# Kernel tuning notes

Measured on AMD Instinct MI355X. Metric: run time of the kernel, lower is better.

Reference implementation:

```python
import jax, jax.numpy as jnp
import numpy as np

D_MODEL = 256
N_HEADS = 4
D_HEAD = D_MODEL // N_HEADS
SCALE = 1.0 / np.sqrt(D_HEAD).astype(np.float32)


def setup_inputs() -> dict:
    key = jax.random.key(0)
    ks = jax.random.split(key, 8)
    B, T, S = 4, 512, 512
    return {
        "query": jax.random.normal(ks[0], (B, T, D_MODEL), dtype=jnp.float32),
        "key": jax.random.normal(ks[1], (B, S, D_MODEL), dtype=jnp.float32),
        "value": jax.random.normal(ks[2], (B, S, D_MODEL), dtype=jnp.float32),
        "w_q": jax.random.normal(ks[3], (D_MODEL, D_MODEL), dtype=jnp.float32) * 0.05,
        "w_k": jax.random.normal(ks[4], (D_MODEL, D_MODEL), dtype=jnp.float32) * 0.05,
        "w_v": jax.random.normal(ks[5], (D_MODEL, D_MODEL), dtype=jnp.float32) * 0.05,
        "v_a": jax.random.normal(ks[6], (N_HEADS, D_HEAD), dtype=jnp.float32),
        "w_o": jax.random.normal(ks[7], (D_MODEL, D_MODEL), dtype=jnp.float32) * 0.05,
    }


def reference(query, key, value, w_q, w_k, w_v, v_a, w_o):
    B, T, _ = query.shape
    S = key.shape[1]
    # projections; weights stored as (out, in) like nn.Linear -> x @ W.T
    Q = (query @ w_q.T).reshape(B, T, N_HEADS, D_HEAD).transpose(0, 2, 1, 3)  # bhtd
    K = (key @ w_k.T).reshape(B, S, N_HEADS, D_HEAD).transpose(0, 2, 1, 3)    # bhsd
    V = (value @ w_v.T).reshape(B, S, N_HEADS, D_HEAD).transpose(0, 2, 1, 3)  # bhsd
    # additive (Bahdanau) scores: tanh broadcast of shape (B,H,T,S,Dh)
    combined = jnp.tanh(Q[:, :, :, None, :] + K[:, :, None, :, :])
    scores = jnp.einsum('bhtsd,hd->bhts', combined, v_a) * SCALE
    attn = jax.nn.softmax(scores, axis=-1)  # (B,H,T,S)
    attended = jnp.einsum('bhts,bhsd->bhtd', attn, V)
    attended = attended.transpose(0, 2, 1, 3).reshape(B, T, D_MODEL)
    out = attended @ w_o.T
    return out, attn
```

## Files before the change

### kernel.cpp

```cpp
#include <hip/hip_runtime.h>
#include <math.h>

#define BATCH 4
#define TLEN 512
#define SLEN 512
#define DM 256
#define NH 4
#define DH 64
#define BT (BATCH * TLEN)

__device__ __forceinline__ float rcp_fast(float x) { return __builtin_amdgcn_rcpf(x); }

__global__ __launch_bounds__(256) void transposeN_kernel(
    const float* __restrict__ s0, const float* __restrict__ s1,
    const float* __restrict__ s2, const float* __restrict__ s3,
    float* __restrict__ d0, float* __restrict__ d1,
    float* __restrict__ d2, float* __restrict__ d3) {
  __shared__ float tile[64][65];
  int m = blockIdx.y;
  const float* S = (m == 0) ? s0 : (m == 1) ? s1 : (m == 2) ? s2 : s3;
  float* D = (m == 0) ? d0 : (m == 1) ? d1 : (m == 2) ? d2 : d3;
  int bx = blockIdx.x;
  int to = (bx & 3) * 64;
  int tk = (bx >> 2) * 64;
  int lo = threadIdx.x >> 6;
  int lk = threadIdx.x & 63;
#pragma unroll
  for (int p = 0; p < 16; ++p) {
    int o = p * 4 + lo;
    tile[o][lk] = S[(size_t)(to + o) * DM + tk + lk];
  }
  __syncthreads();
#pragma unroll
  for (int p = 0; p < 16; ++p) {
    int kk = p * 4 + lo;
    D[(size_t)(tk + kk) * DM + to + lk] = tile[lk][kk];
  }
}

__global__ __launch_bounds__(256) void proj_kernel(
    const float* __restrict__ q, const float* __restrict__ k, const float* __restrict__ v,
    const float* __restrict__ wqt, const float* __restrict__ wkt, const float* __restrict__ wvt,
    float* __restrict__ EQ, float* __restrict__ EKT, float* __restrict__ Vw) {
  int tid = threadIdx.x;
  int lane = tid & 63;
  int wid = __builtin_amdgcn_readfirstlane(tid >> 6);
  int which = blockIdx.y;
  const float* X = (which == 0) ? q : (which == 1) ? k : v;
  const float* WT = (which == 0) ? wqt : (which == 1) ? wkt : wvt;
  int row0 = (blockIdx.x >> 2) * 16 + wid * 4;
  int o = (blockIdx.x & 3) * 64 + lane;
  const float* xb = X + (size_t)row0 * DM;
  const float* wcol = WT + o;
  float a0 = 0.f, a1 = 0.f, a2 = 0.f, a3 = 0.f;
#pragma unroll 8
  for (int kk = 0; kk < DM; ++kk) {
    float w = wcol[(size_t)kk * DM];
    a0 = fmaf(xb[kk], w, a0);
    a1 = fmaf(xb[DM + kk], w, a1);
    a2 = fmaf(xb[2 * DM + kk], w, a2);
    a3 = fmaf(xb[3 * DM + kk], w, a3);
  }
  int h = o >> 6, d = o & 63;
  float accs[4] = {a0, a1, a2, a3};
#pragma unroll
  for (int r = 0; r < 4; ++r) {
    int row = row0 + r;
    int b = row >> 9, t = row & 511;
    int bh = b * NH + h;
    float val = accs[r];
    if (which < 2) {
      val = __expf(2.f * fminf(fmaxf(val, -5.5f), 5.5f));
    }
    if (which == 0) {
      EQ[((size_t)bh * TLEN + t) * DH + d] = val;
    } else if (which == 1) {
      EKT[(((size_t)bh * 16 + (d >> 2)) * SLEN + t) * 4 + (d & 3)] = val;
    } else {
      Vw[(size_t)bh * SLEN * DH + (size_t)(t >> 1) * 128 + d * 2 + (t & 1)] = val;
    }
  }
}

__global__ __launch_bounds__(256, 8) void attn_kernel(
    const float* __restrict__ EQ, const float* __restrict__ EKT,
    const float* __restrict__ Vw, const float* __restrict__ va_g,
    float* __restrict__ attn_out, float* __restrict__ attended) {
  __shared__ float pw[4][SLEN];
  __shared__ float fp[4][4][64];
  __shared__ float sred[4][4];
  int tid = threadIdx.x;
  int lane = tid & 63;
  int wid = __builtin_amdgcn_readfirstlane(tid >> 6);
  int bx = (int)((blockIdx.x & 7) * 256 + (blockIdx.x >> 3));
  int bh = bx >> 7;
  int tile = (bx & 127) * 4;
  int h = bh & 3, b = bh >> 2;
  int sq0 = wid * 128;

  const float4* ekf = (const float4*)EKT + (size_t)bh * (16 * SLEN) + sq0 + lane;
  const float* eqb = EQ + ((size_t)bh * TLEN + tile) * DH;
  const float* vap = va_g + h * DH;

  float acc[4][2];
#pragma unroll
  for (int t = 0; t < 4; ++t) { acc[t][0] = 0.f; acc[t][1] = 0.f; }
  float vsum = 0.f;

  float4 eA0, eA1, eB0, eB1;

#define LOADE(EV, dc_) do { EV##0 = ekf[(size_t)(dc_) * SLEN]; \
                            EV##1 = ekf[(size_t)(dc_) * SLEN + 64]; } while (0)

#define SC4(E, qv, av, aref) do {                                           \
    float A0 = fmaf(qv.x, E.x, 1.f), A1 = fmaf(qv.y, E.y, 1.f);             \
    float A2 = fmaf(qv.z, E.z, 1.f), A3 = fmaf(qv.w, E.w, 1.f);             \
    float n01 = fmaf(av.x, A1, av.y * A0);                                  \
    float n23 = fmaf(av.z, A3, av.w * A2);                                  \
    float P01 = A0 * A1, P23 = A2 * A3;                                     \
    float Nm = fmaf(n01, P23, n23 * P01);                                   \
    aref = fmaf(Nm, rcp_fast(P01 * P23), aref);                             \
  } while (0)

#define DCBODY(CUR, NXT, dc_) do {                                          \
    float4 av = *(const float4*)(vap + (dc_) * 4);                          \
    float4 q0 = *(const float4*)(eqb + 0 * DH + (dc_) * 4);                 \
    float4 q1 = *(const float4*)(eqb + 1 * DH + (dc_) * 4);                 \
    float4 q2 = *(const float4*)(eqb + 2 * DH + (dc_) * 4);                 \
    float4 q3 = *(const float4*)(eqb + 3 * DH + (dc_) * 4);                 \
    vsum += (av.x + av.y) + (av.z + av.w);                                  \
    if ((dc_) < 15) LOADE(NXT, (dc_) + 1);                                  \
    __builtin_amdgcn_sched_barrier(0);                                      \
    SC4(CUR##0, q0, av, acc[0][0]); SC4(CUR##1, q0, av, acc[0][1]);         \
    SC4(CUR##0, q1, av, acc[1][0]); SC4(CUR##1, q1, av, acc[1][1]);         \
    SC4(CUR##0, q2, av, acc[2][0]); SC4(CUR##1, q2, av, acc[2][1]);         \
    SC4(CUR##0, q3, av, acc[3][0]); SC4(CUR##1, q3, av, acc[3][1]);         \
  } while (0)

  LOADE(eA, 0);
#pragma unroll 1
  for (int dc2 = 0; dc2 < 8; ++dc2) {
    DCBODY(eA, eB, 2 * dc2);
    DCBODY(eB, eA, 2 * dc2 + 1);
  }

  size_t bht = (size_t)bh * TLEN + tile;
  float e0[4], e1[4];
#pragma unroll
  for (int t = 0; t < 4; ++t) {
    float x0 = __expf(fmaf(acc[t][0], -0.25f, vsum * 0.125f));
    float x1 = __expf(fmaf(acc[t][1], -0.25f, vsum * 0.125f));
    e0[t] = x0; e1[t] = x1;
    float es = x0 + x1;
#pragma unroll
    for (int off = 32; off; off >>= 1) es += __shfl_xor(es, off);
    if (lane == 0) sred[t][wid] = es;
  }
  __syncthreads();
#pragma unroll
  for (int t = 0; t < 4; ++t) {
    float es = (sred[t][0] + sred[t][1]) + (sred[t][2] + sred[t][3]);
    float inv = rcp_fast(es);
    float p0 = e0[t] * inv, p1 = e1[t] * inv;
    pw[t][sq0 + lane] = p0;
    pw[t][sq0 + 64 + lane] = p1;
    float* arow = attn_out + (bht + t) * SLEN + sq0;
    arow[lane] = p0;
    arow[64 + lane] = p1;
  }

  const float2* vb = (const float2*)Vw + (size_t)bh * (256 * 64) + (size_t)(wid * 64) * 64 + lane;
  float f[4];
#pragma unroll
  for (int t = 0; t < 4; ++t) f[t] = 0.f;
#pragma unroll 2
  for (int i = 0; i < 32; ++i) {
    float2 v01 = vb[(size_t)i * 128];
    float2 v23 = vb[(size_t)i * 128 + 64];
    int sb = sq0 + i * 4;
#pragma unroll
    for (int t = 0; t < 4; ++t) {
      float4 pq = *(const float4*)&pw[t][sb];
      f[t] = fmaf(pq.x, v01.x, f[t]);
      f[t] = fmaf(pq.y, v01.y, f[t]);
      f[t] = fmaf(pq.z, v23.x, f[t]);
      f[t] = fmaf(pq.w, v23.y, f[t]);
    }
  }
#pragma unroll
  for (int t = 0; t < 4; ++t) fp[wid][t][lane] = f[t];
  __syncthreads();
  {
    int t = wid;
    float s = (fp[0][t][lane] + fp[1][t][lane]) + (fp[2][t][lane] + fp[3][t][lane]);
    attended[((size_t)(b * TLEN) + tile + t) * DM + h * DH + lane] = s;
  }
}

__global__ __launch_bounds__(256) void outproj_kernel(
    const float* __restrict__ att, const float* __restrict__ wot,
    float* __restrict__ out) {
  int tid = threadIdx.x;
  int lane = tid & 63;
  int wid = __builtin_amdgcn_readfirstlane(tid >> 6);
  int row0 = (blockIdx.x >> 2) * 8 + wid * 2;
  int o = (blockIdx.x & 3) * 64 + lane;
  const float* xb = att + (size_t)row0 * DM;
  const float* wcol = wot + o;
  float a0 = 0.f, a1 = 0.f;
#pragma unroll 8
  for (int kk = 0; kk < DM; ++kk) {
    float w = wcol[(size_t)kk * DM];
    a0 = fmaf(xb[kk], w, a0);
    a1 = fmaf(xb[DM + kk], w, a1);
  }
  out[(size_t)(row0 + 0) * DM + o] = a0;
  out[(size_t)(row0 + 1) * DM + o] = a1;
}

extern "C" void kernel_launch(void* const* d_in, const int* in_sizes, int n_in,
                              void* d_out, int out_size, void* d_ws, size_t ws_size,
                              hipStream_t stream) {
  const float* query = (const float*)d_in[0];
  const float* key   = (const float*)d_in[1];
  const float* value = (const float*)d_in[2];
  const float* wq    = (const float*)d_in[3];
  const float* wk    = (const float*)d_in[4];
  const float* wv    = (const float*)d_in[5];
  const float* va    = (const float*)d_in[6];
  const float* wo    = (const float*)d_in[7];

  float* out  = (float*)d_out;
  float* attn = out + (size_t)BT * DM;

  const size_t SEG = (size_t)BT * DM;
  float* EQ  = (float*)d_ws;
  float* EKT = EQ + SEG;
  float* Vw  = EKT + SEG;
  float* att = Vw + SEG;

  bool big_ws = ws_size >= (4 * SEG + 4 * (size_t)DM * DM) * sizeof(float);

  if (big_ws) {
    float* WTq = att + SEG;
    float* WTk = WTq + (size_t)DM * DM;
    float* WTv = WTk + (size_t)DM * DM;
    float* WoT = WTv + (size_t)DM * DM;
    transposeN_kernel<<<dim3(16, 4), 256, 0, stream>>>(wq, wk, wv, wo, WTq, WTk, WTv, WoT);
    proj_kernel<<<dim3(512, 3), 256, 0, stream>>>(query, key, value, WTq, WTk, WTv, EQ, EKT, Vw);
    attn_kernel<<<dim3(2048), 256, 0, stream>>>(EQ, EKT, Vw, va, attn, att);
    outproj_kernel<<<dim3(1024), 256, 0, stream>>>(att, WoT, out);
  } else {
    float* WTq = att;
    float* WTk = att + (size_t)DM * DM;
    float* WTv = att + 2 * (size_t)DM * DM;
    float* WoT = EQ;
    transposeN_kernel<<<dim3(16, 3), 256, 0, stream>>>(wq, wk, wv, wv, WTq, WTk, WTv, WTv);
    proj_kernel<<<dim3(512, 3), 256, 0, stream>>>(query, key, value, WTq, WTk, WTv, EQ, EKT, Vw);
    attn_kernel<<<dim3(2048), 256, 0, stream>>>(EQ, EKT, Vw, va, attn, att);
    transposeN_kernel<<<dim3(16, 1), 256, 0, stream>>>(wo, wo, wo, wo, WoT, WoT, WoT, WoT);
    outproj_kernel<<<dim3(1024), 256, 0, stream>>>(att, WoT, out);
  }
}
```

Baseline: 87.14 us.

## Pack exp(K) pairs in interleaved layout and use packed f32x2 math in score loop

The exp(2K) tensor is now stored so that each lane's two key positions (s and s+64) sit next to each other per head-dim element. The score inner loop computes both keys together with 2-wide float vector FMAs/multiplies, targeting the packed FP32 instructions (v_pk_fma_f32, v_pk_mul_f32) available on CDNA3-class GPUs and roughly halving the VALU instruction count for that math. Reciprocals stay scalar. The trade-offs are possible register/packing overhead, since the scalar q/va values must be broadcast into both halves, and a changed global load pattern of 8-byte loads instead of float4.

```diff
diff --git a/kernel.cpp b/kernel.cpp
--- a/kernel.cpp
+++ b/kernel.cpp
@@ -9,16 +9,20 @@
 #define DH 64
 #define BT (BATCH * TLEN)
 
+typedef float f2 __attribute__((ext_vector_type(2)));
+
 __device__ __forceinline__ float rcp_fast(float x) { return __builtin_amdgcn_rcpf(x); }
+__device__ __forceinline__ f2 f2fma(f2 a, f2 b, f2 c) { return __builtin_elementwise_fma(a, b, c); }
+__device__ __forceinline__ f2 s2(float v) { f2 r; r.x = v; r.y = v; return r; }
 
 __global__ __launch_bounds__(256) void transposeN_kernel(
     const float* __restrict__ s0, const float* __restrict__ s1,
-    const float* __restrict__ s2, const float* __restrict__ s3,
+    const float* __restrict__ s2_, const float* __restrict__ s3,
     float* __restrict__ d0, float* __restrict__ d1,
     float* __restrict__ d2, float* __restrict__ d3) {
   __shared__ float tile[64][65];
   int m = blockIdx.y;
-  const float* S = (m == 0) ? s0 : (m == 1) ? s1 : (m == 2) ? s2 : s3;
+  const float* S = (m == 0) ? s0 : (m == 1) ? s1 : (m == 2) ? s2_ : s3;
   float* D = (m == 0) ? d0 : (m == 1) ? d1 : (m == 2) ? d2 : d3;
   int bx = blockIdx.x;
   int to = (bx & 3) * 64;
@@ -75,7 +79,8 @@
     if (which == 0) {
       EQ[((size_t)bh * TLEN + t) * DH + d] = val;
     } else if (which == 1) {
-      EKT[(((size_t)bh * 16 + (d >> 2)) * SLEN + t) * 4 + (d & 3)] = val;
+      int dc = d >> 2, j = d & 3, qq = t >> 7, l = t & 63, hi = (t >> 6) & 1;
+      EKT[((((size_t)bh * 16 + dc) * 4 + qq) * 64 + l) * 8 + j * 2 + hi] = val;
     } else {
       Vw[(size_t)bh * SLEN * DH + (size_t)(t >> 1) * 128 + d * 2 + (t & 1)] = val;
     }
@@ -98,58 +103,64 @@
   int h = bh & 3, b = bh >> 2;
   int sq0 = wid * 128;
 
-  const float4* ekf = (const float4*)EKT + (size_t)bh * (16 * SLEN) + sq0 + lane;
+  const float* ekb = EKT + (size_t)bh * (16 * 2048) + wid * 512 + lane * 8;
   const float* eqb = EQ + ((size_t)bh * TLEN + tile) * DH;
   const float* vap = va_g + h * DH;
 
-  float acc[4][2];
-#pragma unroll
-  for (int t = 0; t < 4; ++t) { acc[t][0] = 0.f; acc[t][1] = 0.f; }
+  f2 acc2[4];
+#pragma unroll
+  for (int t = 0; t < 4; ++t) acc2[t] = s2(0.f);
   float vsum = 0.f;
 
-  float4 eA0, eA1, eB0, eB1;
-
-#define LOADE(EV, dc_) do { EV##0 = ekf[(size_t)(dc_) * SLEN]; \
-                            EV##1 = ekf[(size_t)(dc_) * SLEN + 64]; } while (0)
-
-#define SC4(E, qv, av, aref) do {                                           \
-    float A0 = fmaf(qv.x, E.x, 1.f), A1 = fmaf(qv.y, E.y, 1.f);             \
-    float A2 = fmaf(qv.z, E.z, 1.f), A3 = fmaf(qv.w, E.w, 1.f);             \
-    float n01 = fmaf(av.x, A1, av.y * A0);                                  \
-    float n23 = fmaf(av.z, A3, av.w * A2);                                  \
-    float P01 = A0 * A1, P23 = A2 * A3;                                     \
-    float Nm = fmaf(n01, P23, n23 * P01);                                   \
-    aref = fmaf(Nm, rcp_fast(P01 * P23), aref);                             \
+  f2 a0_, a1_, a2_, a3_, b0_, b1_, b2_, b3_;
+
+#define LOADP(E0, E1, E2, E3, dc_) do {                                     \
+    const f2* _p = (const f2*)(ekb + (size_t)(dc_) * 2048);                 \
+    E0 = _p[0]; E1 = _p[1]; E2 = _p[2]; E3 = _p[3];                         \
   } while (0)
 
-#define DCBODY(CUR, NXT, dc_) do {                                          \
+#define SC4P(E0, E1, E2, E3, qv, av, aref) do {                             \
+    f2 A0 = f2fma(s2(qv.x), E0, s2(1.f));                                   \
+    f2 A1 = f2fma(s2(qv.y), E1, s2(1.f));                                   \
+    f2 A2 = f2fma(s2(qv.z), E2, s2(1.f));                                   \
+    f2 A3 = f2fma(s2(qv.w), E3, s2(1.f));                                   \
+    f2 n01 = f2fma(s2(av.x), A1, s2(av.y) * A0);                            \
+    f2 n23 = f2fma(s2(av.z), A3, s2(av.w) * A2);                            \
+    f2 P01 = A0 * A1, P23 = A2 * A3;                                        \
+    f2 Nm = f2fma(n01, P23, n23 * P01);                                     \
+    f2 PP = P01 * P23;                                                      \
+    f2 R; R.x = rcp_fast(PP.x); R.y = rcp_fast(PP.y);                       \
+    aref = f2fma(Nm, R, aref);                                              \
+  } while (0)
+
+#define DCBODYP(C0, C1, C2, C3, N0, N1, N2, N3, dc_) do {                   \
     float4 av = *(const float4*)(vap + (dc_) * 4);                          \
     float4 q0 = *(const float4*)(eqb + 0 * DH + (dc_) * 4);                 \
     float4 q1 = *(const float4*)(eqb + 1 * DH + (dc_) * 4);                 \
     float4 q2 = *(const float4*)(eqb + 2 * DH + (dc_) * 4);                 \
     float4 q3 = *(const float4*)(eqb + 3 * DH + (dc_) * 4);                 \
     vsum += (av.x + av.y) + (av.z + av.w);                                  \
-    if ((dc_) < 15) LOADE(NXT, (dc_) + 1);                                  \
+    if ((dc_) < 15) LOADP(N0, N1, N2, N3, (dc_) + 1);                       \
     __builtin_amdgcn_sched_barrier(0);                                      \
-    SC4(CUR##0, q0, av, acc[0][0]); SC4(CUR##1, q0, av, acc[0][1]);         \
-    SC4(CUR##0, q1, av, acc[1][0]); SC4(CUR##1, q1, av, acc[1][1]);         \
-    SC4(CUR##0, q2, av, acc[2][0]); SC4(CUR##1, q2, av, acc[2][1]);         \
-    SC4(CUR##0, q3, av, acc[3][0]); SC4(CUR##1, q3, av, acc[3][1]);         \
+    SC4P(C0, C1, C2, C3, q0, av, acc2[0]);                                  \
+    SC4P(C0, C1, C2, C3, q1, av, acc2[1]);                                  \
+    SC4P(C0, C1, C2, C3, q2, av, acc2[2]);                                  \
+    SC4P(C0, C1, C2, C3, q3, av, acc2[3]);                                  \
   } while (0)
 
-  LOADE(eA, 0);
+  LOADP(a0_, a1_, a2_, a3_, 0);
 #pragma unroll 1
   for (int dc2 = 0; dc2 < 8; ++dc2) {
-    DCBODY(eA, eB, 2 * dc2);
-    DCBODY(eB, eA, 2 * dc2 + 1);
+    DCBODYP(a0_, a1_, a2_, a3_, b0_, b1_, b2_, b3_, 2 * dc2);
+    DCBODYP(b0_, b1_, b2_, b3_, a0_, a1_, a2_, a3_, 2 * dc2 + 1);
   }
 
   size_t bht = (size_t)bh * TLEN + tile;
   float e0[4], e1[4];
 #pragma unroll
   for (int t = 0; t < 4; ++t) {
-    float x0 = __expf(fmaf(acc[t][0], -0.25f, vsum * 0.125f));
-    float x1 = __expf(fmaf(acc[t][1], -0.25f, vsum * 0.125f));
+    float x0 = __expf(fmaf(acc2[t].x, -0.25f, vsum * 0.125f));
+    float x1 = __expf(fmaf(acc2[t].y, -0.25f, vsum * 0.125f));
     e0[t] = x0; e1[t] = x1;
     float es = x0 + x1;
 #pragma unroll
```

Result: no change. 86.80 us (median of 2 runs) (-0.4%).
